# Kernel optimization log

Hardware: AMD Instinct MI355X
Metric: run time of the kernel (lower is better)

## Reference

```python
import jax, jax.numpy as jnp
import numpy as np

BATCH = 1024
M = 64      # N_v measurements
N = 8192    # N_theta unknowns
STEPS = 3   # N_admm_steps
EPS_DIV = 1e-12


def setup_inputs() -> dict:
    key = jax.random.key(0)
    k = jax.random.split(key, 4)
    return {
        "r_n": jax.random.normal(k[0], (BATCH, 2, N), jnp.float32),
        "y": jax.random.normal(k[1], (BATCH, 2, M), jnp.float32),
        "u_in": jax.random.normal(k[2], (BATCH, 2, M), jnp.float32),
        "A": jax.random.normal(k[3], (2, M, N), jnp.float32) / np.sqrt(N).astype(np.float32),
        "log_rho": jnp.zeros((), jnp.float32),                 # rho = 1.0
        "log_epsilon": jnp.asarray(np.log(0.01), jnp.float32), # epsilon = 0.01
    }


def _cmm(Ar, Ai, v):
    # complex matmul A @ v : v [b,2,N] -> [b,2,M]
    vr, vi = v[:, 0], v[:, 1]
    return jnp.stack([vr @ Ar.T - vi @ Ai.T, vi @ Ar.T + vr @ Ai.T], axis=1)


def _chm(Ar, Ai, v):
    # complex conj-transpose matmul A^H @ v : v [b,2,M] -> [b,2,N]
    vr, vi = v[:, 0], v[:, 1]
    return jnp.stack([vr @ Ar + vi @ Ai, vi @ Ar - vr @ Ai], axis=1)


def reference(r_n, y, u_in, A, log_rho, log_epsilon):
    rho = jnp.exp(log_rho)
    epsilon = jnp.exp(log_epsilon)
    Ar, Ai = A[0], A[1]  # [M, N]

    # SMW system matrix: S = (1/rho) I + A A^H, written as real 2Mx2M block matrix.
    # It is constant across ADMM steps (rho fixed within a forward pass).
    I_M = jnp.eye(M, dtype=A.dtype)
    S_r = I_M / (rho + EPS_DIV) + Ar @ Ar.T + Ai @ Ai.T
    S_i = Ai @ Ar.T - Ar @ Ai.T
    S_block = jnp.block([[S_r, -S_i], [S_i, S_r]])  # [2M, 2M]

    x, z, u = r_n, y, u_in
    for _ in range(STEPS):
        # x-update via SMW: x = b - A^H (S^{-1} A b), b = r_n + rho A^H (z - u)
        b = r_n + rho * _chm(Ar, Ai, z - u)          # [b,2,N]
        Ab = _cmm(Ar, Ai, b)                          # [b,2,M]
        R = jnp.concatenate([Ab[:, 0], Ab[:, 1]], axis=1)  # [b,2M]
        sol = jnp.linalg.solve(S_block, R.T)          # [2M, b]
        T = jnp.stack([sol[:M].T, sol[M:].T], axis=1)  # [b,2,M]
        x = b - _chm(Ar, Ai, T)                       # [b,2,N]
        # enforce_real: zero imaginary part; enforce_positivity: clamp real part
        x = jnp.stack([jnp.maximum(x[:, 0], 0.0), jnp.zeros_like(x[:, 0])], axis=1)
        # z-update: project residual onto complex L2 ball of radius epsilon
        Ax = _cmm(Ar, Ai, x)                          # [b,2,M]
        v = Ax + u - y
        nrm = jnp.sqrt(jnp.sum(v * v, axis=(1, 2), keepdims=True))
        z = y + v * jnp.minimum(1.0, epsilon / (nrm + EPS_DIV))
        # dual update
        u = u + Ax - z
    return x, u
```

## Files before the change

kernel.cpp:

```cpp
#include <hip/hip_runtime.h>

#define B_ 1024
#define M_ 64
#define N_ 8192
#define NSG 16
#define NS3 8

typedef __attribute__((ext_vector_type(8))) short bf16x8;
typedef __attribute__((ext_vector_type(4))) float f32x4;

__device__ inline unsigned short f2b(float f) {
    union { float f; unsigned u; } v; v.f = f;
    unsigned r = v.u + 0x7FFFu + ((v.u >> 16) & 1u);
    return (unsigned short)(r >> 16);
}
__device__ inline unsigned rne2(float lo, float hi) {
    union { float f; unsigned u; } a, b; a.f = lo; b.f = hi;
    unsigned x = (a.u + 0x7FFFu + ((a.u >> 16) & 1u)) >> 16;
    unsigned y = (b.u + 0x7FFFu + ((b.u >> 16) & 1u)) >> 16;
    return x | (y << 16);
}
__device__ inline float b2f(unsigned short s) {
    union { unsigned u; float f; } v; v.u = ((unsigned)s) << 16; return v.f;
}
__device__ inline float rl(float v, int l) {
    return __builtin_bit_cast(float, __builtin_amdgcn_readlane(__builtin_bit_cast(int, v), l));
}

__global__ __launch_bounds__(256) void k_cvt(const float* src, unsigned short* dst) {
    size_t i = ((size_t)blockIdx.x * 256 + threadIdx.x) * 8;
    float4 f0 = *(const float4*)(src + i);
    float4 f1 = *(const float4*)(src + i + 4);
    union { bf16x8 v; unsigned u[4]; } r;
    r.u[0] = rne2(f0.x, f0.y); r.u[1] = rne2(f0.z, f0.w);
    r.u[2] = rne2(f1.x, f1.y); r.u[3] = rne2(f1.z, f1.w);
    *(bf16x8*)(dst + i) = r.v;
}

__global__ __launch_bounds__(256) void k_prep(const float* A, unsigned short* Abf,
                                              unsigned short* WgT, unsigned short* ATb) {
    __shared__ float tile[128][65];
    int n0 = blockIdx.x * 64;
    int t = threadIdx.x;
    int nl = t % 64, r0 = t / 64;
#pragma unroll
    for (int it = 0; it < 32; ++it) {
        int row = r0 + it * 4;
        tile[row][nl] = A[(size_t)row * N_ + n0 + nl];
    }
    __syncthreads();
#pragma unroll
    for (int it = 0; it < 32; ++it) {
        int row = r0 + it * 4;
        float v = tile[row][nl];
        unsigned short bv = f2b(v);
        Abf[(size_t)row * N_ + n0 + nl] = bv;
        if (row < 64) {
            WgT[(size_t)row * 16384 + n0 + nl] = bv;
            WgT[(size_t)(64 + row) * 16384 + 8192 + n0 + nl] = bv;
        } else {
            int m = row - 64;
            WgT[(size_t)m * 16384 + 8192 + n0 + nl] = f2b(-v);
            WgT[(size_t)(64 + m) * 16384 + n0 + nl] = bv;
        }
    }
    int o = t % 128, nn0 = t / 128;
#pragma unroll
    for (int it = 0; it < 32; ++it) {
        int nn = nn0 + it * 2;
        ATb[(size_t)(n0 + nn) * 128 + o] = f2b(tile[o][nn]);
    }
}

__global__ __launch_bounds__(256) void k_Sbuild(const float* A, const float* lr,
                                                float* S, float* AAHT) {
    __shared__ float redS[8];
    int bid = blockIdx.x;
    int i = 0, rem = bid;
    while (rem >= 64 - i) { rem -= 64 - i; ++i; }
    int j = i + rem;
    int t = threadIdx.x;
    const float* Ar = A;
    const float* Ai = A + (size_t)M_ * N_;
    const float* ari = Ar + (size_t)i * N_;
    const float* aii = Ai + (size_t)i * N_;
    const float* arj = Ar + (size_t)j * N_;
    const float* aij = Ai + (size_t)j * N_;
    float aR = 0.f, aI = 0.f;
#pragma unroll
    for (int it = 0; it < 8; ++it) {
        int n = it * 1024 + t * 4;
        float4 xr = *(const float4*)(ari + n);
        float4 xi = *(const float4*)(aii + n);
        float4 br = *(const float4*)(arj + n);
        float4 bi = *(const float4*)(aij + n);
        aR += xr.x * br.x + xi.x * bi.x + xr.y * br.y + xi.y * bi.y
            + xr.z * br.z + xi.z * bi.z + xr.w * br.w + xi.w * bi.w;
        aI += xi.x * br.x - xr.x * bi.x + xi.y * br.y - xr.y * bi.y
            + xi.z * br.z - xr.z * bi.z + xi.w * br.w - xr.w * bi.w;
    }
    for (int off = 32; off > 0; off >>= 1) {
        aR += __shfl_down(aR, off, 64);
        aI += __shfl_down(aI, off, 64);
    }
    int lane = t & 63, w = t >> 6;
    if (lane == 0) { redS[w * 2] = aR; redS[w * 2 + 1] = aI; }
    __syncthreads();
    if (t == 0) {
        float R = redS[0] + redS[2] + redS[4] + redS[6];
        float I = redS[1] + redS[3] + redS[5] + redS[7];
        float inv_rho = 1.0f / (expf(lr[0]) + 1e-12f);
        float diag = (i == j) ? inv_rho : 0.f;
        S[((size_t)i * 64 + j) * 2 + 0] = R + diag;
        S[((size_t)i * 64 + j) * 2 + 1] = I;
        AAHT[((size_t)j * 64 + i) * 2 + 0] = R;
        AAHT[((size_t)j * 64 + i) * 2 + 1] = I;
        if (i != j) {
            S[((size_t)j * 64 + i) * 2 + 0] = R;
            S[((size_t)j * 64 + i) * 2 + 1] = -I;
            AAHT[((size_t)i * 64 + j) * 2 + 0] = R;
            AAHT[((size_t)i * 64 + j) * 2 + 1] = -I;
        }
    }
}

__global__ __launch_bounds__(256, 2) void k_Ginv(const unsigned short* rnb,
                                                 const unsigned short* WgT,
                                                 float* Gpart,
                                                 const float* S, float* Wt) {
    int t = threadIdx.x;
    int lane = t & 63;
    if (blockIdx.x == 0) {
        __shared__ float2 Tp[2][16][64];
        int g = t >> 6;
        float mx0,my0,mx1,my1,mx2,my2,mx3,my3,mx4,my4,mx5,my5,mx6,my6,mx7,my7;
        float mx8,my8,mx9,my9,mx10,my10,mx11,my11,mx12,my12,mx13,my13,mx14,my14,mx15,my15;
#define GJ_INIT(J) { int c = 16 * g + (J);                                   \
    float2 v = ((const float2*)S)[(size_t)lane * 64 + c];                    \
    mx##J = v.x; my##J = v.y; }
        GJ_INIT(0) GJ_INIT(1) GJ_INIT(2) GJ_INIT(3) GJ_INIT(4) GJ_INIT(5) GJ_INIT(6) GJ_INIT(7)
        GJ_INIT(8) GJ_INIT(9) GJ_INIT(10) GJ_INIT(11) GJ_INIT(12) GJ_INIT(13) GJ_INIT(14) GJ_INIT(15)
#undef GJ_INIT

#define FUP(J, j) if ((J) != (j)) {                                          \
    float sx = rl(mx##J, k), sy = rl(my##J, k);                              \
    float nx = a * mx##J - (fpx * sx - fpy * sy);                            \
    float ny = a * my##J - (fpx * sy + fpy * sx);                            \
    mx##J = nx; my##J = ny; }
#define FACT_STEP(j) {                                                       \
    int k = 16 * p + (j);                                                    \
    float px = rl(mx##j, k), py = rl(my##j, k);                              \
    float d = px * px + py * py;                                             \
    float id = 1.0f / d;                                                     \
    float pix = px * id, piy = -py * id;                                     \
    bool isk = (lane == k);                                                  \
    float a   = isk ? 0.f : 1.f;                                             \
    float fpx = isk ? -pix : (mx##j * pix - my##j * piy);                    \
    float fpy = isk ? -piy : (mx##j * piy + my##j * pix);                    \
    FUP(0, j) FUP(1, j) FUP(2, j) FUP(3, j) FUP(4, j) FUP(5, j) FUP(6, j) FUP(7, j) \
    FUP(8, j) FUP(9, j) FUP(10, j) FUP(11, j) FUP(12, j) FUP(13, j) FUP(14, j) FUP(15, j) \
    mx##j = -fpx; my##j = -fpy; }

        for (int p = 0; p < 4; ++p) {
            const int buf = p & 1;
            if (g == p) {
                FACT_STEP(0)  FACT_STEP(1)  FACT_STEP(2)  FACT_STEP(3)
                FACT_STEP(4)  FACT_STEP(5)  FACT_STEP(6)  FACT_STEP(7)
                FACT_STEP(8)  FACT_STEP(9)  FACT_STEP(10) FACT_STEP(11)
                FACT_STEP(12) FACT_STEP(13) FACT_STEP(14) FACT_STEP(15)
#define GJ_PUB(J) Tp[buf][J][lane] = make_float2(mx##J, my##J);
                GJ_PUB(0) GJ_PUB(1) GJ_PUB(2) GJ_PUB(3) GJ_PUB(4) GJ_PUB(5) GJ_PUB(6) GJ_PUB(7)
                GJ_PUB(8) GJ_PUB(9) GJ_PUB(10) GJ_PUB(11) GJ_PUB(12) GJ_PUB(13) GJ_PUB(14) GJ_PUB(15)
#undef GJ_PUB
            }
            __syncthreads();
            if (g != p) {
#define TL(j) float tx##j = Tp[buf][j][lane].x, ty##j = Tp[buf][j][lane].y;
                TL(0) TL(1) TL(2) TL(3) TL(4) TL(5) TL(6) TL(7)
                TL(8) TL(9) TL(10) TL(11) TL(12) TL(13) TL(14) TL(15)
#undef TL
                float msk = ((lane >> 4) == p) ? 0.f : 1.f;
#define TFMA(j, J) { float sx = rl(mx##J, 16 * p + (j)), sy = rl(my##J, 16 * p + (j)); \
    ax += tx##j * sx - ty##j * sy; ay += tx##j * sy + ty##j * sx; }
#define TRAIL_COL(J) { float ax = msk * mx##J, ay = msk * my##J;             \
    TFMA(0, J) TFMA(1, J) TFMA(2, J) TFMA(3, J) TFMA(4, J) TFMA(5, J) TFMA(6, J) TFMA(7, J) \
    TFMA(8, J) TFMA(9, J) TFMA(10, J) TFMA(11, J) TFMA(12, J) TFMA(13, J) TFMA(14, J) TFMA(15, J) \
    mx##J = ax; my##J = ay; }
                TRAIL_COL(0)  TRAIL_COL(1)  TRAIL_COL(2)  TRAIL_COL(3)
                TRAIL_COL(4)  TRAIL_COL(5)  TRAIL_COL(6)  TRAIL_COL(7)
                TRAIL_COL(8)  TRAIL_COL(9)  TRAIL_COL(10) TRAIL_COL(11)
                TRAIL_COL(12) TRAIL_COL(13) TRAIL_COL(14) TRAIL_COL(15)
#undef TRAIL_COL
#undef TFMA
            }
        }
#undef FACT_STEP
#undef FUP
#define GJ_OUT(J) { int c = 16 * g + (J);                                    \
    ((float2*)Wt)[(size_t)c * 64 + lane] = make_float2(mx##J, my##J); }
        GJ_OUT(0) GJ_OUT(1) GJ_OUT(2) GJ_OUT(3) GJ_OUT(4) GJ_OUT(5) GJ_OUT(6) GJ_OUT(7)
        GJ_OUT(8) GJ_OUT(9) GJ_OUT(10) GJ_OUT(11) GJ_OUT(12) GJ_OUT(13) GJ_OUT(14) GJ_OUT(15)
#undef GJ_OUT
        return;
    }
    int bx = blockIdx.x - 1;
    int w = t >> 6;
    int l15 = lane & 15;
    int q8 = (lane >> 4) * 8;
    int split = bx & 15;
    int b0 = (bx >> 4) * 16;
    int k0 = split * 1024;
    f32x4 a00 = {}, a01 = {};
    const unsigned short* x0 = rnb + (size_t)(b0 + l15) * 16384 + k0 + q8;
    const unsigned short* w0 = WgT + (size_t)(w * 32 + l15) * 16384 + k0 + q8;
    const unsigned short* w1 = w0 + (size_t)16 * 16384;
#pragma unroll 8
    for (int ks = 0; ks < 32; ++ks) {
        int kk = ks * 32;
        bf16x8 af0 = *(const bf16x8*)(x0 + kk);
        bf16x8 bf0 = *(const bf16x8*)(w0 + kk);
        bf16x8 bf1 = *(const bf16x8*)(w1 + kk);
        a00 = __builtin_amdgcn_mfma_f32_16x16x32_bf16(af0, bf0, a00, 0, 0, 0);
        a01 = __builtin_amdgcn_mfma_f32_16x16x32_bf16(af0, bf1, a01, 0, 0, 0);
    }
    int row = (lane >> 4) * 4;
    size_t base = (size_t)split * (B_ * 128);
    float* g = Gpart + base + (size_t)(b0 + row) * 128 + w * 32 + l15;
#pragma unroll
    for (int r = 0; r < 4; ++r) {
        g[(size_t)r * 128] = a00[r];
        g[(size_t)r * 128 + 16] = a01[r];
    }
}

__global__ __launch_bounds__(256) void k_small12(const float* Gpart, const float* AAHT,
                                                 const float* Wt, const float* zin,
                                                 const float* uin, const float* lr,
                                                 unsigned short* qb) {
    __shared__ float2 AbS[4][64];
    int t = threadIdx.x;
    int m = t & 63;
    int w = __builtin_amdgcn_readfirstlane(t >> 6);
    int b = blockIdx.x * 4 + w;
    float rho = expf(lr[0]);
    float abR = 0.f, abI = 0.f;
    for (int k = 0; k < 64; ++k) {
        float wr = zin[(b * 2 + 0) * 64 + k] - uin[(b * 2 + 0) * 64 + k];
        float wi = zin[(b * 2 + 1) * 64 + k] - uin[(b * 2 + 1) * 64 + k];
        float2 h = *(const float2*)(AAHT + ((size_t)k * 64 + m) * 2);
        abR += wr * h.x - wi * h.y;
        abI += wi * h.x + wr * h.y;
    }
    float gR = 0.f, gI = 0.f;
#pragma unroll
    for (int s = 0; s < NSG; ++s) {
        gR += Gpart[(size_t)s * 131072 + (size_t)b * 128 + m];
        gI += Gpart[(size_t)s * 131072 + (size_t)b * 128 + 64 + m];
    }
    abR = gR + rho * abR;
    abI = gI + rho * abI;
    AbS[w][m] = make_float2(abR, abI);
    __syncthreads();
    float tR = 0.f, tI = 0.f;
    for (int k = 0; k < 64; ++k) {
        float2 Wv = *(const float2*)(Wt + ((size_t)k * 64 + m) * 2);
        float2 ab = AbS[w][k];
        tR += ab.x * Wv.x - ab.y * Wv.y;
        tI += ab.y * Wv.x + ab.x * Wv.y;
    }
    float wr_m = zin[(b * 2 + 0) * 64 + m] - uin[(b * 2 + 0) * 64 + m];
    float wi_m = zin[(b * 2 + 1) * 64 + m] - uin[(b * 2 + 1) * 64 + m];
    qb[(size_t)b * 128 + m] = f2b(rho * wr_m - tR);
    qb[(size_t)b * 128 + 64 + m] = f2b(rho * wi_m - tI);
}

__global__ __launch_bounds__(256, 3) void k_H23(const unsigned short* qb, const unsigned short* ATb,
                                                const unsigned short* rnb, const unsigned short* Abf,
                                                float* out, float* Axpart, int last) {
    __shared__ __align__(16) char lds_buf[4 * 8448];
    int t = threadIdx.x;
    int lane = t & 63;
    int w = t >> 6;
    int l15 = lane & 15;
    int q8 = (lane >> 4) * 8;
    int row = (lane >> 4) * 4;
    int slab = blockIdx.x;
    int b0 = blockIdx.y * 16;
    int n0 = slab * 1024 + w * 256;
    short* xs = (short*)(lds_buf + w * 8448);
    float* rs = (float*)(lds_buf + w * 8448);

    bf16x8 a[4];
    const unsigned short* qrow = qb + (size_t)(b0 + l15) * 128 + q8;
#pragma unroll
    for (int ks = 0; ks < 4; ++ks) a[ks] = *(const bf16x8*)(qrow + ks * 32);
#pragma unroll 2
    for (int nt = 0; nt < 16; ++nt) {
        f32x4 acc = {};
        const unsigned short* bbase = ATb + (size_t)(n0 + nt * 16 + l15) * 128 + q8;
#pragma unroll
        for (int ks = 0; ks < 4; ++ks) {
            bf16x8 bf = *(const bf16x8*)(bbase + ks * 32);
            acc = __builtin_amdgcn_mfma_f32_16x16x32_bf16(a[ks], bf, acc, 0, 0, 0);
        }
        int ncol = n0 + nt * 16 + l15;
        int nloc = nt * 16 + l15;
#pragma unroll
        for (int r = 0; r < 4; ++r) {
            size_t ridx = (size_t)(b0 + row + r) * 16384 + ncol;
            float v = fmaxf(acc[r] + b2f(rnb[ridx]), 0.f);
            if (last) out[ridx] = v;
            xs[(row + r) * 264 + nloc] = (short)f2b(v);
        }
    }
    f32x4 acc8[8] = {};
#pragma unroll
    for (int ks = 0; ks < 8; ++ks) {
        bf16x8 xf = *(const bf16x8*)(xs + l15 * 264 + ks * 32 + q8);
#pragma unroll
        for (int ot = 0; ot < 8; ++ot) {
            const unsigned short* bp = Abf + (size_t)(ot * 16 + l15) * 8192 + n0 + ks * 32 + q8;
            acc8[ot] = __builtin_amdgcn_mfma_f32_16x16x32_bf16(xf, *(const bf16x8*)bp, acc8[ot], 0, 0, 0);
        }
    }
    __syncthreads();
#pragma unroll
    for (int ot = 0; ot < 8; ++ot)
#pragma unroll
        for (int r = 0; r < 4; ++r)
            rs[(row + r) * 132 + ot * 16 + l15] = acc8[ot][r];
    __syncthreads();
#pragma unroll
    for (int e = t; e < 2048; e += 256) {
        int b = e >> 7, o = e & 127;
        float sAx = 0.f;
#pragma unroll
        for (int ww = 0; ww < 4; ++ww)
            sAx += ((const float*)(lds_buf + ww * 8448))[b * 132 + o];
        Axpart[(size_t)slab * 131072 + (size_t)(b0 + b) * 128 + o] = sAx;
    }
    if (last) {
        float4 z4 = make_float4(0.f, 0.f, 0.f, 0.f);
        for (int e = t; e < 4096; e += 256) {
            int bb = e >> 8, nq = e & 255;
            *(float4*)(out + ((size_t)(b0 + bb) * 2 + 1) * N_ + slab * 1024 + nq * 4) = z4;
        }
    }
}

__global__ __launch_bounds__(128) void k_small3(const float* Axpart, const float* uin,
                                                const float* y, const float* le,
                                                float* z, float* u, float* uout, int last) {
    __shared__ float red[2];
    int b = blockIdx.x, t = threadIdx.x;
    size_t idx = (size_t)b * 128 + t;
    float ax = 0.f;
#pragma unroll
    for (int s = 0; s < NS3; ++s) ax += Axpart[(size_t)s * 131072 + idx];
    float uo = uin[idx], yv = y[idx];
    float v = ax + uo - yv;
    float sq = v * v;
    for (int off = 32; off > 0; off >>= 1) sq += __shfl_down(sq, off, 64);
    if ((t & 63) == 0) red[t >> 6] = sq;
    __syncthreads();
    float tot = red[0] + red[1];
    float eps = expf(le[0]);
    float scale = fminf(1.f, eps / (sqrtf(tot) + 1e-12f));
    float zv = yv + v * scale;
    float un = uo + ax - zv;
    z[idx] = zv;
    u[idx] = un;
    if (last) uout[idx] = un;
}

extern "C" void kernel_launch(void* const* d_in, const int* in_sizes, int n_in,
                              void* d_out, int out_size, void* d_ws, size_t ws_size,
                              hipStream_t stream) {
    const float* rn  = (const float*)d_in[0];
    const float* y   = (const float*)d_in[1];
    const float* uin = (const float*)d_in[2];
    const float* A   = (const float*)d_in[3];
    const float* lr  = (const float*)d_in[4];
    const float* le  = (const float*)d_in[5];

    float* out = (float*)d_out;
    float* ws  = (float*)d_ws;

    float* Gpart  = ws;
    float* Axpart = Gpart + (size_t)NSG * 131072;
    float* S      = Axpart + (size_t)NS3 * 131072;
    float* AAHT   = S + 8192;
    float* Wt     = AAHT + 8192;
    float* z      = Wt + 8192;
    float* u      = z + 131072;
    unsigned short* qb  = (unsigned short*)(u + 131072);
    unsigned short* rnb = qb + 131072;
    unsigned short* WgT = rnb + (size_t)B_ * 16384;
    unsigned short* Abf = WgT + 2097152;
    unsigned short* ATb = Abf + 1048576;
    float* uout = out + (size_t)B_ * 2 * N_;

    k_prep<<<128, 256, 0, stream>>>(A, Abf, WgT, ATb);
    k_cvt<<<8192, 256, 0, stream>>>(rn, rnb);
    k_Sbuild<<<2080, 256, 0, stream>>>(A, lr, S, AAHT);
    k_Ginv<<<1025, 256, 0, stream>>>(rnb, WgT, Gpart, S, Wt);

    for (int step = 0; step < 3; ++step) {
        const float* zp = (step == 0) ? y   : z;
        const float* up = (step == 0) ? uin : u;
        int last = (step == 2) ? 1 : 0;
        k_small12<<<256, 256, 0, stream>>>(Gpart, AAHT, Wt, zp, up, lr, qb);
        k_H23<<<dim3(NS3, 64), 256, 0, stream>>>(qb, ATb, rnb, Abf, out, Axpart, last);
        k_small3<<<B_, 128, 0, stream>>>(Axpart, up, y, le, z, u, uout, last);
    }
}
```

Before: 420.8 us.

## Cyclically distribute Gauss-Jordan panels and fold inversion into a GEMM block

The matrix inversion in block 0 now uses 4-column panels distributed cyclically across the four waves, instead of one 16-column panel per wave. Every wave does trailing updates every round, so fewer waves sit idle while one factors. Block 0 no longer returns after the inversion: it raises its wave priority and then also computes a GEMM tile, which removes the extra block from the grid. The cost is 16 barrier rounds instead of 4, and block 0's GEMM tile will finish late.

```diff
diff --git a/kernel.cpp b/kernel.cpp
--- a/kernel.cpp
+++ b/kernel.cpp
@@ -131,79 +131,97 @@
     int t = threadIdx.x;
     int lane = t & 63;
     if (blockIdx.x == 0) {
-        __shared__ float2 Tp[2][16][64];
+        __builtin_amdgcn_s_setprio(1);
+        __shared__ float2 Tp[2][4][64];
         int g = t >> 6;
         float mx0,my0,mx1,my1,mx2,my2,mx3,my3,mx4,my4,mx5,my5,mx6,my6,mx7,my7;
         float mx8,my8,mx9,my9,mx10,my10,mx11,my11,mx12,my12,mx13,my13,mx14,my14,mx15,my15;
-#define GJ_INIT(J) { int c = 16 * g + (J);                                   \
+#define GJ_INIT(J) { int c = 16 * ((J) >> 2) + 4 * g + ((J) & 3);            \
     float2 v = ((const float2*)S)[(size_t)lane * 64 + c];                    \
     mx##J = v.x; my##J = v.y; }
         GJ_INIT(0) GJ_INIT(1) GJ_INIT(2) GJ_INIT(3) GJ_INIT(4) GJ_INIT(5) GJ_INIT(6) GJ_INIT(7)
         GJ_INIT(8) GJ_INIT(9) GJ_INIT(10) GJ_INIT(11) GJ_INIT(12) GJ_INIT(13) GJ_INIT(14) GJ_INIT(15)
 #undef GJ_INIT
 
-#define FUP(J, j) if ((J) != (j)) {                                          \
-    float sx = rl(mx##J, k), sy = rl(my##J, k);                              \
-    float nx = a * mx##J - (fpx * sx - fpy * sy);                            \
-    float ny = a * my##J - (fpx * sy + fpy * sx);                            \
-    mx##J = nx; my##J = ny; }
-#define FACT_STEP(j) {                                                       \
-    int k = 16 * p + (j);                                                    \
-    float px = rl(mx##j, k), py = rl(my##j, k);                              \
+#define PIV(JA, JB0, JB1, JB2, jj) {                                         \
+    int k = p4 + (jj);                                                       \
+    float px = rl(mx##JA, k), py = rl(my##JA, k);                            \
     float d = px * px + py * py;                                             \
     float id = 1.0f / d;                                                     \
     float pix = px * id, piy = -py * id;                                     \
     bool isk = (lane == k);                                                  \
     float a   = isk ? 0.f : 1.f;                                             \
-    float fpx = isk ? -pix : (mx##j * pix - my##j * piy);                    \
-    float fpy = isk ? -piy : (mx##j * piy + my##j * pix);                    \
-    FUP(0, j) FUP(1, j) FUP(2, j) FUP(3, j) FUP(4, j) FUP(5, j) FUP(6, j) FUP(7, j) \
-    FUP(8, j) FUP(9, j) FUP(10, j) FUP(11, j) FUP(12, j) FUP(13, j) FUP(14, j) FUP(15, j) \
-    mx##j = -fpx; my##j = -fpy; }
-
-        for (int p = 0; p < 4; ++p) {
+    float fpx = isk ? -pix : (mx##JA * pix - my##JA * piy);                  \
+    float fpy = isk ? -piy : (mx##JA * piy + my##JA * pix);                  \
+    { float sx = rl(mx##JB0, k), sy = rl(my##JB0, k);                        \
+      float nx = a * mx##JB0 - (fpx * sx - fpy * sy);                        \
+      float ny = a * my##JB0 - (fpx * sy + fpy * sx);                        \
+      mx##JB0 = nx; my##JB0 = ny; }                                          \
+    { float sx = rl(mx##JB1, k), sy = rl(my##JB1, k);                        \
+      float nx = a * mx##JB1 - (fpx * sx - fpy * sy);                        \
+      float ny = a * my##JB1 - (fpx * sy + fpy * sx);                        \
+      mx##JB1 = nx; my##JB1 = ny; }                                          \
+    { float sx = rl(mx##JB2, k), sy = rl(my##JB2, k);                        \
+      float nx = a * mx##JB2 - (fpx * sx - fpy * sy);                        \
+      float ny = a * my##JB2 - (fpx * sy + fpy * sx);                        \
+      mx##JB2 = nx; my##JB2 = ny; }                                          \
+    mx##JA = -fpx; my##JA = -fpy; }
+
+#define FACT4(J0, J1, J2, J3) {                                              \
+    PIV(J0, J1, J2, J3, 0) PIV(J1, J0, J2, J3, 1)                            \
+    PIV(J2, J0, J1, J3, 2) PIV(J3, J0, J1, J2, 3)                            \
+    Tp[buf][0][lane] = make_float2(mx##J0, my##J0);                          \
+    Tp[buf][1][lane] = make_float2(mx##J1, my##J1);                          \
+    Tp[buf][2][lane] = make_float2(mx##J2, my##J2);                          \
+    Tp[buf][3][lane] = make_float2(mx##J3, my##J3); }
+
+        for (int p = 0; p < 16; ++p) {
             const int buf = p & 1;
-            if (g == p) {
-                FACT_STEP(0)  FACT_STEP(1)  FACT_STEP(2)  FACT_STEP(3)
-                FACT_STEP(4)  FACT_STEP(5)  FACT_STEP(6)  FACT_STEP(7)
-                FACT_STEP(8)  FACT_STEP(9)  FACT_STEP(10) FACT_STEP(11)
-                FACT_STEP(12) FACT_STEP(13) FACT_STEP(14) FACT_STEP(15)
-#define GJ_PUB(J) Tp[buf][J][lane] = make_float2(mx##J, my##J);
-                GJ_PUB(0) GJ_PUB(1) GJ_PUB(2) GJ_PUB(3) GJ_PUB(4) GJ_PUB(5) GJ_PUB(6) GJ_PUB(7)
-                GJ_PUB(8) GJ_PUB(9) GJ_PUB(10) GJ_PUB(11) GJ_PUB(12) GJ_PUB(13) GJ_PUB(14) GJ_PUB(15)
-#undef GJ_PUB
+            const int p4  = p * 4;
+            const int q   = p >> 2;
+            const bool own = (g == (p & 3));
+            if (own) {
+                switch (q) {
+                    case 0:  FACT4(0, 1, 2, 3)     break;
+                    case 1:  FACT4(4, 5, 6, 7)     break;
+                    case 2:  FACT4(8, 9, 10, 11)   break;
+                    default: FACT4(12, 13, 14, 15) break;
+                }
             }
             __syncthreads();
-            if (g != p) {
-#define TL(j) float tx##j = Tp[buf][j][lane].x, ty##j = Tp[buf][j][lane].y;
-                TL(0) TL(1) TL(2) TL(3) TL(4) TL(5) TL(6) TL(7)
-                TL(8) TL(9) TL(10) TL(11) TL(12) TL(13) TL(14) TL(15)
-#undef TL
-                float msk = ((lane >> 4) == p) ? 0.f : 1.f;
-#define TFMA(j, J) { float sx = rl(mx##J, 16 * p + (j)), sy = rl(my##J, 16 * p + (j)); \
-    ax += tx##j * sx - ty##j * sy; ay += tx##j * sy + ty##j * sx; }
-#define TRAIL_COL(J) { float ax = msk * mx##J, ay = msk * my##J;             \
-    TFMA(0, J) TFMA(1, J) TFMA(2, J) TFMA(3, J) TFMA(4, J) TFMA(5, J) TFMA(6, J) TFMA(7, J) \
-    TFMA(8, J) TFMA(9, J) TFMA(10, J) TFMA(11, J) TFMA(12, J) TFMA(13, J) TFMA(14, J) TFMA(15, J) \
+            float2 t0 = Tp[buf][0][lane];
+            float2 t1 = Tp[buf][1][lane];
+            float2 t2 = Tp[buf][2][lane];
+            float2 t3 = Tp[buf][3][lane];
+            float msk = ((lane >> 2) == p) ? 0.f : 1.f;
+            int skipq = own ? q : -1;
+#define TRAIL(J) if (((J) >> 2) != skipq) {                                  \
+    float s0x = rl(mx##J, p4),     s0y = rl(my##J, p4);                      \
+    float s1x = rl(mx##J, p4 + 1), s1y = rl(my##J, p4 + 1);                  \
+    float s2x = rl(mx##J, p4 + 2), s2y = rl(my##J, p4 + 2);                  \
+    float s3x = rl(mx##J, p4 + 3), s3y = rl(my##J, p4 + 3);                  \
+    float ax = msk * mx##J, ay = msk * my##J;                                \
+    ax += t0.x * s0x - t0.y * s0y; ay += t0.x * s0y + t0.y * s0x;            \
+    ax += t1.x * s1x - t1.y * s1y; ay += t1.x * s1y + t1.y * s1x;            \
+    ax += t2.x * s2x - t2.y * s2y; ay += t2.x * s2y + t2.y * s2x;            \
+    ax += t3.x * s3x - t3.y * s3y; ay += t3.x * s3y + t3.y * s3x;            \
     mx##J = ax; my##J = ay; }
-                TRAIL_COL(0)  TRAIL_COL(1)  TRAIL_COL(2)  TRAIL_COL(3)
-                TRAIL_COL(4)  TRAIL_COL(5)  TRAIL_COL(6)  TRAIL_COL(7)
-                TRAIL_COL(8)  TRAIL_COL(9)  TRAIL_COL(10) TRAIL_COL(11)
-                TRAIL_COL(12) TRAIL_COL(13) TRAIL_COL(14) TRAIL_COL(15)
-#undef TRAIL_COL
-#undef TFMA
-            }
-        }
-#undef FACT_STEP
-#undef FUP
-#define GJ_OUT(J) { int c = 16 * g + (J);                                    \
+            TRAIL(0)  TRAIL(1)  TRAIL(2)  TRAIL(3)
+            TRAIL(4)  TRAIL(5)  TRAIL(6)  TRAIL(7)
+            TRAIL(8)  TRAIL(9)  TRAIL(10) TRAIL(11)
+            TRAIL(12) TRAIL(13) TRAIL(14) TRAIL(15)
+#undef TRAIL
+        }
+#undef FACT4
+#undef PIV
+#define GJ_OUT(J) { int c = 16 * ((J) >> 2) + 4 * g + ((J) & 3);             \
     ((float2*)Wt)[(size_t)c * 64 + lane] = make_float2(mx##J, my##J); }
         GJ_OUT(0) GJ_OUT(1) GJ_OUT(2) GJ_OUT(3) GJ_OUT(4) GJ_OUT(5) GJ_OUT(6) GJ_OUT(7)
         GJ_OUT(8) GJ_OUT(9) GJ_OUT(10) GJ_OUT(11) GJ_OUT(12) GJ_OUT(13) GJ_OUT(14) GJ_OUT(15)
 #undef GJ_OUT
-        return;
-    }
-    int bx = blockIdx.x - 1;
+        __builtin_amdgcn_s_setprio(0);
+    }
+    int bx = blockIdx.x;
     int w = t >> 6;
     int l15 = lane & 15;
     int q8 = (lane >> 4) * 8;
@@ -403,7 +421,7 @@
     k_prep<<<128, 256, 0, stream>>>(A, Abf, WgT, ATb);
     k_cvt<<<8192, 256, 0, stream>>>(rn, rnb);
     k_Sbuild<<<2080, 256, 0, stream>>>(A, lr, S, AAHT);
-    k_Ginv<<<1025, 256, 0, stream>>>(rnb, WgT, Gpart, S, Wt);
+    k_Ginv<<<1024, 256, 0, stream>>>(rnb, WgT, Gpart, S, Wt);
 
     for (int step = 0; step < 3; ++step) {
         const float* zp = (step == 0) ? y   : z;
```

After: 356.1 us. 1.18x faster.
